# Performance work log

Hardware: AMD Instinct MI355X
Metric: run time of the kernel (lower is better)

Reference implementation:

```python
import jax, jax.numpy as jnp
import numpy as np

B, S, D, H = 2, 2048, 1024, 16
DK = D // H  # 64
ROPE_BASE = 10000.0


def _rope_tables(dk, seq_len, base=ROPE_BASE):
    inv_freq = 1.0 / base ** (jnp.arange(0, dk, 2, dtype=jnp.float32) / dk)
    t = jnp.arange(seq_len, dtype=jnp.float32)
    freqs = t[:, None] * inv_freq[None, :]            # [S, dk/2]
    cos = jnp.repeat(jnp.cos(freqs), 2, axis=-1)      # [S, dk] (repeat_interleave)
    sin = jnp.repeat(jnp.sin(freqs), 2, axis=-1)
    return cos, sin


def _rotate_half(x):
    x1, x2 = jnp.split(x, 2, axis=-1)
    return jnp.concatenate((-x2, x1), axis=-1)


def setup_inputs() -> dict:
    key = jax.random.key(0)
    ks = jax.random.split(key, 9)
    scale = 0.02
    x = jax.random.normal(ks[0], (B, S, D), jnp.float32)
    wq = jax.random.normal(ks[1], (D, D), jnp.float32) * scale
    wk = jax.random.normal(ks[2], (D, D), jnp.float32) * scale
    wv = jax.random.normal(ks[3], (D, D), jnp.float32) * scale
    wo = jax.random.normal(ks[4], (D, D), jnp.float32) * scale
    bq = jnp.zeros((D,), jnp.float32)
    bk = jnp.zeros((D,), jnp.float32)
    bv = jnp.zeros((D,), jnp.float32)
    bo = jnp.zeros((D,), jnp.float32)
    mask = jnp.tril(jnp.ones((S, S), dtype=bool))[None, None]  # [1,1,S,S] causal
    return {"x": x, "mask": mask, "wq": wq, "bq": bq, "wk": wk, "bk": bk,
            "wv": wv, "bv": bv, "wo": wo, "bo": bo}


def reference(x, mask, wq, bq, wk, bk, wv, bv, wo, bo):
    b, s, d = x.shape
    h, dk = H, DK
    # QKV projections (nn.Linear: x @ W^T + b), split heads -> [B,H,S,dk]
    q = (x @ wq.T + bq).reshape(b, s, h, dk).transpose(0, 2, 1, 3)
    k = (x @ wk.T + bk).reshape(b, s, h, dk).transpose(0, 2, 1, 3)
    v = (x @ wv.T + bv).reshape(b, s, h, dk).transpose(0, 2, 1, 3)
    # RoPE
    cos, sin = _rope_tables(dk, s)                    # [S, dk]
    cos = cos[None, None]                             # [1,1,S,dk]
    sin = sin[None, None]
    q = q * cos + _rotate_half(q) * sin
    k = k * cos + _rotate_half(k) * sin
    # Naive attention: full [B,H,S,S] scores
    scores = jnp.einsum("bhqd,bhkd->bhqk", q, k) / np.float32(np.sqrt(dk))
    scores = jnp.where(mask, scores, jnp.float32(-1e9))
    attn = jax.nn.softmax(scores, axis=-1)
    out = jnp.einsum("bhqk,bhkd->bhqd", attn, v)      # [B,H,S,dk]
    out = out.transpose(0, 2, 1, 3).reshape(b, s, d)  # [B,S,D]
    return out @ wo.T + bo
```

## Files before the change

### kernel.cpp

```cpp
#include <hip/hip_runtime.h>
#include <hip/hip_bf16.h>

#define B_ 2
#define S_ 2048
#define D_ 1024
#define H_ 16
#define DK_ 64
#define BH_ (B_*H_)

typedef __attribute__((ext_vector_type(8))) short short8;
typedef __attribute__((ext_vector_type(4))) short short4v;
typedef __attribute__((ext_vector_type(4))) float f32x4;

__device__ __forceinline__ unsigned short f2bf(float f) {
  unsigned u = __float_as_uint(f);
  u += 0x7FFFu + ((u >> 16) & 1u);
  return (unsigned short)(u >> 16);
}
__device__ __forceinline__ float bf2f(unsigned short b) {
  return __uint_as_float(((unsigned)b) << 16);
}
__device__ __forceinline__ unsigned pk2bf(float lo, float hi) {
  float2 f; f.x = lo; f.y = hi;
  __hip_bfloat162 t = __float22bfloat162_rn(f);
  unsigned r; __builtin_memcpy(&r, &t, 4); return r;
}
__device__ __forceinline__ float fexp2(float x) {
  float r; asm("v_exp_f32 %0, %1" : "=v"(r) : "v"(x)); return r;
}

__device__ __forceinline__ long ftile_off(int n, int k, int ktiles) {
  return ((long)(n >> 7) * ktiles + (k >> 5)) * 4096 + ((k >> 3) & 3) * 1024 + (n & 127) * 8 + (k & 7);
}

__global__ __launch_bounds__(256) void cvt_kernel(const float* __restrict__ x, const float* __restrict__ wq,
                           const float* __restrict__ wk, const float* __restrict__ wv,
                           const float* __restrict__ wo, const float* __restrict__ bq,
                           const float* __restrict__ bk, const float* __restrict__ bv,
                           unsigned short* __restrict__ xb, unsigned short* __restrict__ wqkvb,
                           unsigned short* __restrict__ wob, float* __restrict__ bqkv,
                           float* __restrict__ ctab) {
  const int bi = blockIdx.x;
  if (bi >= 2051) {
    const int idx = (bi - 2051) * 256 + (int)threadIdx.x;
    const int s = idx >> 5, j = idx & 31;
    const float invf = fexp2((float)j * -0.4152410118609203f);
    float sn, cc;
    __sincosf((float)s * invf, &sn, &cc);
    ctab[(long)idx * 2] = cc;
    ctab[(long)idx * 2 + 1] = sn;
    return;
  }
  if (bi >= 2048) {
    const int i = (bi - 2048) * 1024 + (int)threadIdx.x * 4;
    const float* bb = (i < D_) ? (bq + i) : ((i < 2 * D_) ? (bk + i - D_) : (bv + i - 2 * D_));
    *(float4*)(bqkv + i) = *(const float4*)bb;
    return;
  }
  __shared__ alignas(16) unsigned short lt[4096];
  const int t = threadIdx.x;
  const int r = t >> 1, kb = (t & 1) * 16;
  int ti; unsigned short* dst;
  if (bi < 1024) { ti = bi; dst = xb; }
  else if (bi < 1792) { ti = bi - 1024; dst = wqkvb; }
  else { ti = bi - 1792; dst = wob; }
  const int rt = ti >> 5, kt = ti & 31;
  const int grow = rt * 128 + r;
  const float* sp;
  if (bi < 1024) sp = x + (long)grow * 1024 + kt * 32 + kb;
  else if (bi < 1792) {
    const float* w = (grow < 1024) ? wq : ((grow < 2048) ? wk : wv);
    sp = w + (long)(grow & 1023) * 1024 + kt * 32 + kb;
  } else sp = wo + (long)grow * 1024 + kt * 32 + kb;

  const float4 va = ((const float4*)sp)[0], vb = ((const float4*)sp)[1];
  const float4 vc = ((const float4*)sp)[2], vd = ((const float4*)sp)[3];
  short8 o0, o1;
  o0[0] = f2bf(va.x); o0[1] = f2bf(va.y); o0[2] = f2bf(va.z); o0[3] = f2bf(va.w);
  o0[4] = f2bf(vb.x); o0[5] = f2bf(vb.y); o0[6] = f2bf(vb.z); o0[7] = f2bf(vb.w);
  o1[0] = f2bf(vc.x); o1[1] = f2bf(vc.y); o1[2] = f2bf(vc.z); o1[3] = f2bf(vc.w);
  o1[4] = f2bf(vd.x); o1[5] = f2bf(vd.y); o1[6] = f2bf(vd.z); o1[7] = f2bf(vd.w);
  const int kc0 = kb >> 3;
  *(short8*)(lt + kc0 * 1024 + r * 8) = o0;
  *(short8*)(lt + (kc0 + 1) * 1024 + r * 8) = o1;
  __syncthreads();
  unsigned short* dp = dst + ((long)rt * 32 + kt) * 4096 + t * 16;
  *(short8*)dp       = *(const short8*)(lt + t * 16);
  *(short8*)(dp + 8) = *(const short8*)(lt + t * 16 + 8);
}

__global__ __launch_bounds__(256) void gemm_qkv(const unsigned short* __restrict__ A,
                                                const unsigned short* __restrict__ Bm,
                                                const float* __restrict__ bias,
                                                const float* __restrict__ ctab,
                                                unsigned short* __restrict__ Qh,
                                                unsigned short* __restrict__ Kf,
                                                unsigned short* __restrict__ Vf) {
  __shared__ alignas(16) unsigned short As[4096];
  __shared__ alignas(16) unsigned short Bs[4096];
  __shared__ alignas(16) unsigned short epi[4 * 4480];
  const int t = threadIdx.x;
  const int w = t >> 6;
  const int lane = t & 63;
  const int bcol = blockIdx.x * 128;
  const int wr = (w >> 1) * 64, wc = (w & 1) * 64;
  const int fr = lane & 15;
  const int g = lane >> 4;
  const int ktiles = 32;
  f32x4 acc[4][4] = {};

  for (int kt = 0; kt < ktiles; ++kt) {
    const unsigned short* Asrc = A  + ((long)blockIdx.y * ktiles + kt) * 4096;
    const unsigned short* Bsrc = Bm + ((long)blockIdx.x * ktiles + kt) * 4096;
#pragma unroll
    for (int j = 0; j < 2; ++j) {
      const int off = (w * 2 + j) * 512;
      __builtin_amdgcn_global_load_lds((const __attribute__((address_space(1))) void*)(Asrc + off + lane * 8),
                                       (__attribute__((address_space(3))) void*)(As + off), 16, 0, 0);
      __builtin_amdgcn_global_load_lds((const __attribute__((address_space(1))) void*)(Bsrc + off + lane * 8),
                                       (__attribute__((address_space(3))) void*)(Bs + off), 16, 0, 0);
    }
    __syncthreads();
    short8 a[4], b[4];
#pragma unroll
    for (int m = 0; m < 4; ++m)
      a[m] = *(const short8*)(As + g * 1024 + (wr + m * 16 + fr) * 8);
#pragma unroll
    for (int n = 0; n < 4; ++n)
      b[n] = *(const short8*)(Bs + g * 1024 + (wc + n * 16 + fr) * 8);
#pragma unroll
    for (int m = 0; m < 4; ++m)
#pragma unroll
      for (int n = 0; n < 4; ++n)
        acc[m][n] = __builtin_amdgcn_mfma_f32_16x16x32_bf16(a[m], b[n], acc[m][n], 0, 0, 0);
    __syncthreads();
  }

  const int colbase = bcol + wc;
  const int ct = colbase >> 6;
  const int h = ct & 15;
  const int rowbase = blockIdx.y * 128 + wr;
  const int s0 = rowbase & (S_ - 1);
  const int bh = (rowbase >> 11) * 16 + h;
  unsigned short* ep = epi + w * 4480;

#pragma unroll
  for (int n = 0; n < 4; ++n) {
    const int d = n * 16 + fr;
    const float bb = bias[colbase + d];
#pragma unroll
    for (int m = 0; m < 4; ++m)
#pragma unroll
      for (int i = 0; i < 4; ++i)
        ep[(m * 16 + g * 4 + i) * 70 + d] = f2bf(acc[m][n][i] + bb);
  }

  if (ct < 32) {
    const bool isQ = (ct < 16);
    const int s = s0 + lane;
    const unsigned short* rp = ep + lane * 70;
    const f32x4* cp4 = (const f32x4*)(ctab + (long)s * 64);
    const float QS = 0.18033688011112043f;
    unsigned short* qp = Qh + (long)bh * (S_ * DK_) + (long)s * DK_;
    unsigned short* kp = Kf + (long)bh * (S_ * DK_) + (long)(s >> 4) * 1024 + (s & 15) * 8;
#pragma unroll
    for (int c = 0; c < 4; ++c) {
      const short8 vlo = *(const short8*)(rp + c * 8);
      const short8 vhi = *(const short8*)(rp + 32 + c * 8);
      const f32x4 tl0 = cp4[c * 2],     tl1 = cp4[c * 2 + 1];
      const f32x4 th0 = cp4[8 + c * 2], th1 = cp4[8 + c * 2 + 1];
      short8 olo, ohi;
#pragma unroll
      for (int e = 0; e < 8; ++e) {
        const int j = e >> 1;
        const float c1 = (j < 2) ? ((j & 1) ? tl0[2] : tl0[0]) : ((j & 1) ? tl1[2] : tl1[0]);
        const float s1 = (j < 2) ? ((j & 1) ? tl0[3] : tl0[1]) : ((j & 1) ? tl1[3] : tl1[1]);
        const float c2 = (j < 2) ? ((j & 1) ? th0[2] : th0[0]) : ((j & 1) ? th1[2] : th1[0]);
        const float s2 = (j < 2) ? ((j & 1) ? th0[3] : th0[1]) : ((j & 1) ? th1[3] : th1[1]);
        const float v1 = bf2f((unsigned short)vlo[e]);
        const float v2 = bf2f((unsigned short)vhi[e]);
        float o1 = v1 * c1 - v2 * s1;
        float o2 = v2 * c2 + v1 * s2;
        if (isQ) { o1 *= QS; o2 *= QS; }
        olo[e] = (short)f2bf(o1);
        ohi[e] = (short)f2bf(o2);
      }
      if (isQ) {
        *(short8*)(qp + c * 8) = olo;
        *(short8*)(qp + 32 + c * 8) = ohi;
      } else {
        *(short8*)(kp + c * 128) = olo;
        *(short8*)(kp + 512 + c * 128) = ohi;
      }
    }
  } else {
#pragma unroll
    for (int c32loc = 0; c32loc < 2; ++c32loc) {
      unsigned short* vb = Vf + ((long)(bh * 64 + (s0 >> 5) + c32loc)) * 2048;
#pragma unroll
      for (int q = 0; q < 4; ++q) {
        const int idx = q * 64 + lane;
        const int tt = idx >> 6, g2 = (idx >> 4) & 3, frd = idx & 15;
        const int d = tt * 16 + frd;
        short8 o;
#pragma unroll
        for (int j = 0; j < 8; ++j) {
          const int r = (j < 4) ? (4 * g2 + j) : (16 + 4 * g2 + (j - 4));
          o[j] = ep[(c32loc * 32 + r) * 70 + d];
        }
        *(short8*)(vb + tt * 512 + g2 * 128 + frd * 8) = o;
      }
    }
  }
}

template<bool OUT_F32>
__global__ __launch_bounds__(256) void gemm_bt(const unsigned short* __restrict__ A,
                                               const unsigned short* __restrict__ Bm,
                                               const float* __restrict__ bias,
                                               void* __restrict__ Cp, int M, int N, int K) {
  __shared__ alignas(16) unsigned short As[4096];
  __shared__ alignas(16) unsigned short Bs[4096];
  const int t = threadIdx.x;
  const int w = t >> 6;
  const int lane = t & 63;
  const int brow = blockIdx.y * 128;
  const int bcol = blockIdx.x * 128;
  const int wr = (w >> 1) * 64, wc = (w & 1) * 64;
  const int fr = lane & 15;
  const int g = lane >> 4;
  const int ktiles = K >> 5;
  f32x4 acc[4][4] = {};

  for (int kt = 0; kt < ktiles; ++kt) {
    const unsigned short* Asrc = A  + ((long)blockIdx.y * ktiles + kt) * 4096;
    const unsigned short* Bsrc = Bm + ((long)blockIdx.x * ktiles + kt) * 4096;
#pragma unroll
    for (int j = 0; j < 2; ++j) {
      const int off = (w * 2 + j) * 512;
      __builtin_amdgcn_global_load_lds((const __attribute__((address_space(1))) void*)(Asrc + off + lane * 8),
                                       (__attribute__((address_space(3))) void*)(As + off), 16, 0, 0);
      __builtin_amdgcn_global_load_lds((const __attribute__((address_space(1))) void*)(Bsrc + off + lane * 8),
                                       (__attribute__((address_space(3))) void*)(Bs + off), 16, 0, 0);
    }
    __syncthreads();
    short8 a[4], b[4];
#pragma unroll
    for (int m = 0; m < 4; ++m)
      a[m] = *(const short8*)(As + g * 1024 + (wr + m * 16 + fr) * 8);
#pragma unroll
    for (int n = 0; n < 4; ++n)
      b[n] = *(const short8*)(Bs + g * 1024 + (wc + n * 16 + fr) * 8);
#pragma unroll
    for (int m = 0; m < 4; ++m)
#pragma unroll
      for (int n = 0; n < 4; ++n)
        acc[m][n] = __builtin_amdgcn_mfma_f32_16x16x32_bf16(a[m], b[n], acc[m][n], 0, 0, 0);
    __syncthreads();
  }

#pragma unroll
  for (int m = 0; m < 4; ++m) {
#pragma unroll
    for (int n = 0; n < 4; ++n) {
      const int col = bcol + wc + n * 16 + fr;
      const float bv_ = bias[col];
#pragma unroll
      for (int i = 0; i < 4; ++i) {
        const int row = brow + wr + m * 16 + g * 4 + i;
        const float v = acc[m][n][i] + bv_;
        if (OUT_F32) ((float*)Cp)[(long)row * N + col] = v;
        else ((unsigned short*)Cp)[(long)row * N + col] = f2bf(v);
      }
    }
  }
}

__global__ __launch_bounds__(256) void flash_kernel(const unsigned short* __restrict__ Qh,
                                                    const unsigned short* __restrict__ Kf,
                                                    const unsigned short* __restrict__ Vf,
                                                    unsigned short* __restrict__ attnout) {
  __shared__ alignas(16) unsigned short Ks[8192];
  __shared__ alignas(16) unsigned short Vs[8192];

  const int flat = (int)blockIdx.x;
  const int xcd = flat & 7;
  const int ix  = flat >> 3;
  const int k   = ix >> 5;
  const int c   = ix & 31;
  const int bh  = xcd * 4 + k;
  const int qblk = (k & 1) ? c : 31 - c;

  const int b = bh >> 4, h = bh & 15;
  const int w = threadIdx.x >> 6, lane = threadIdx.x & 63;
  const int fr = lane & 15, g = lane >> 4;
  const int qg = qblk * 64 + w * 16 + fr;

  const unsigned short* Qb = Qh + (long)bh * (S_ * DK_);
  const short8 qf0 = *(const short8*)(Qb + (long)qg * DK_ + g * 8);
  const short8 qf1 = *(const short8*)(Qb + (long)qg * DK_ + 32 + g * 8);

  short8 vone;
#pragma unroll
  for (int i = 0; i < 8; ++i) vone[i] = (short)0x3F80;

  f32x4 acc[4] = {};
  f32x4 acl = {};

  const unsigned short* kfb = Kf + (long)bh * (S_ * DK_);
  const unsigned short* vfb = Vf + (long)bh * (S_ * DK_);
  const int kvend = qblk * 64;
  const int frag = g * 128 + fr * 8;

  for (int kv0 = 0; kv0 <= kvend; kv0 += 128) {
    {
      const unsigned short* gk = kfb + (long)kv0 * 64 + w * 2048 + lane * 8;
      unsigned short* lk = Ks + w * 2048;
      const unsigned short* gv = vfb + (long)kv0 * 64 + w * 2048 + lane * 8;
      unsigned short* lv = Vs + w * 2048;
#pragma unroll
      for (int cc = 0; cc < 4; ++cc) {
        __builtin_amdgcn_global_load_lds((const __attribute__((address_space(1))) void*)(gk + cc * 512),
                                         (__attribute__((address_space(3))) void*)(lk + cc * 512), 16, 0, 0);
        __builtin_amdgcn_global_load_lds((const __attribute__((address_space(1))) void*)(gv + cc * 512),
                                         (__attribute__((address_space(3))) void*)(lv + cc * 512), 16, 0, 0);
      }
    }
    __syncthreads();
    const bool domask = (kv0 + 128 > kvend);

#pragma unroll
    for (int sub = 0; sub < 2; ++sub) {
      const unsigned short* ksb = Ks + sub * 4096;
      const unsigned short* vsb = Vs + sub * 4096;

      f32x4 st[4];
      __builtin_amdgcn_s_setprio(1);
#pragma unroll
      for (int cc = 0; cc < 4; ++cc) {
        const short8 k0 = *(const short8*)(ksb + cc * 1024 + frag);
        const short8 k1 = *(const short8*)(ksb + cc * 1024 + 512 + frag);
        f32x4 z = {};
        z = __builtin_amdgcn_mfma_f32_16x16x32_bf16(k0, qf0, z, 0, 0, 0);
        z = __builtin_amdgcn_mfma_f32_16x16x32_bf16(k1, qf1, z, 0, 0, 0);
        st[cc] = z;
      }
      __builtin_amdgcn_s_setprio(0);

      if (domask) {
        const int base = kv0 + sub * 64 + g * 4;
#pragma unroll
        for (int cc = 0; cc < 4; ++cc)
#pragma unroll
          for (int i = 0; i < 4; ++i)
            if (base + cc * 16 + i > qg) st[cc][i] = -3.0e38f;
      }

      float ps[16];
#pragma unroll
      for (int cc = 0; cc < 4; ++cc)
#pragma unroll
        for (int i = 0; i < 4; ++i) ps[cc * 4 + i] = fexp2(st[cc][i]);

      union { short8 s8; unsigned u[4]; } P0, P1;
#pragma unroll
      for (int i = 0; i < 4; ++i) {
        P0.u[i] = pk2bf(ps[2 * i], ps[2 * i + 1]);
        P1.u[i] = pk2bf(ps[8 + 2 * i], ps[8 + 2 * i + 1]);
      }

      __builtin_amdgcn_s_setprio(1);
#pragma unroll
      for (int t = 0; t < 4; ++t) {
        const short8 va = *(const short8*)(vsb + t * 512 + frag);
        const short8 vb = *(const short8*)(vsb + 2048 + t * 512 + frag);
        acc[t] = __builtin_amdgcn_mfma_f32_16x16x32_bf16(va, P0.s8, acc[t], 0, 0, 0);
        acc[t] = __builtin_amdgcn_mfma_f32_16x16x32_bf16(vb, P1.s8, acc[t], 0, 0, 0);
      }
      acl = __builtin_amdgcn_mfma_f32_16x16x32_bf16(vone, P0.s8, acl, 0, 0, 0);
      acl = __builtin_amdgcn_mfma_f32_16x16x32_bf16(vone, P1.s8, acl, 0, 0, 0);
      __builtin_amdgcn_s_setprio(0);
    }
    __syncthreads();
  }

  const float ri = 1.0f / acl[0];
  const int row = b * S_ + qg;
#pragma unroll
  for (int t = 0; t < 4; ++t) {
    short4v ov;
#pragma unroll
    for (int i = 0; i < 4; ++i) ov[i] = (short)f2bf(acc[t][i] * ri);
    const int kcol = h * 64 + t * 16 + g * 4;
    *(short4v*)(attnout + ftile_off(row, kcol, 32)) = ov;
  }
}

extern "C" void kernel_launch(void* const* d_in, const int* in_sizes, int n_in,
                              void* d_out, int out_size, void* d_ws, size_t ws_size,
                              hipStream_t stream) {
  const float* x  = (const float*)d_in[0];
  const float* wq = (const float*)d_in[2];
  const float* bq = (const float*)d_in[3];
  const float* wk = (const float*)d_in[4];
  const float* bk = (const float*)d_in[5];
  const float* wv = (const float*)d_in[6];
  const float* bv = (const float*)d_in[7];
  const float* wo = (const float*)d_in[8];
  const float* bo = (const float*)d_in[9];

  const long NX = (long)B_ * S_ * D_;
  const long NW = (long)D_ * D_;

  unsigned short* xb    = (unsigned short*)d_ws;
  unsigned short* wqkvb = xb + NX;
  unsigned short* wob   = wqkvb + 3 * NW;
  float*          bqkv  = (float*)(wob + NW);
  unsigned short* Qh    = (unsigned short*)(bqkv + 3 * D_);
  unsigned short* Kf    = Qh + NX;
  unsigned short* Vf    = Kf + NX;
  float*          ctab  = (float*)(Vf + NX);
  unsigned short* attnout = xb;

  cvt_kernel<<<2307, 256, 0, stream>>>(x, wq, wk, wv, wo, bq, bk, bv,
                                       xb, wqkvb, wob, bqkv, ctab);
  gemm_qkv<<<dim3(24, 32), 256, 0, stream>>>(xb, wqkvb, bqkv, ctab, Qh, Kf, Vf);
  flash_kernel<<<1024, 256, 0, stream>>>(Qh, Kf, Vf, attnout);
  gemm_bt<true><<<dim3(8, 32), 256, 0, stream>>>(attnout, wob, bo, d_out, 4096, 1024, 1024);
}
```

Before: 108.5 us.

## Process two 64-row query tiles per flash block to reuse K/V loads

Each flash-attention block now handles 128 query rows: each wave holds two sets of Q fragments and computes scores for both against every staged K/V chunk. K/V shared-memory traffic per query is halved, and the kernel launches half as many blocks. The grid-to-(bh, qblk) mapping is reworked so long and short causal blocks are paired within an XCD. On the last chunk the A tile skips the second sub-tile, which is fully masked for it. The cost is roughly double the accumulator registers, which may lower occupancy, plus fewer blocks to spread the causal imbalance over.

```diff
diff --git a/kernel.cpp b/kernel.cpp
--- a/kernel.cpp
+++ b/kernel.cpp
@@ -286,33 +286,36 @@
   const int flat = (int)blockIdx.x;
   const int xcd = flat & 7;
   const int ix  = flat >> 3;
-  const int k   = ix >> 5;
+  const int p   = ix >> 5;
   const int c   = ix & 31;
-  const int bh  = xcd * 4 + k;
-  const int qblk = (k & 1) ? c : 31 - c;
+  const int bh  = xcd * 4 + (c & 1) + 2 * p;
+  const int qblk = p ? (15 - (c >> 1)) : (c >> 1);
 
   const int b = bh >> 4, h = bh & 15;
   const int w = threadIdx.x >> 6, lane = threadIdx.x & 63;
   const int fr = lane & 15, g = lane >> 4;
-  const int qg = qblk * 64 + w * 16 + fr;
+  const int qgA = qblk * 128 + w * 16 + fr;
+  const int qgB = qgA + 64;
 
   const unsigned short* Qb = Qh + (long)bh * (S_ * DK_);
-  const short8 qf0 = *(const short8*)(Qb + (long)qg * DK_ + g * 8);
-  const short8 qf1 = *(const short8*)(Qb + (long)qg * DK_ + 32 + g * 8);
+  const short8 qA0 = *(const short8*)(Qb + (long)qgA * DK_ + g * 8);
+  const short8 qA1 = *(const short8*)(Qb + (long)qgA * DK_ + 32 + g * 8);
+  const short8 qB0 = *(const short8*)(Qb + (long)qgB * DK_ + g * 8);
+  const short8 qB1 = *(const short8*)(Qb + (long)qgB * DK_ + 32 + g * 8);
 
   short8 vone;
 #pragma unroll
   for (int i = 0; i < 8; ++i) vone[i] = (short)0x3F80;
 
-  f32x4 acc[4] = {};
-  f32x4 acl = {};
+  f32x4 accA[4] = {}, accB[4] = {};
+  f32x4 aclA = {}, aclB = {};
 
   const unsigned short* kfb = Kf + (long)bh * (S_ * DK_);
   const unsigned short* vfb = Vf + (long)bh * (S_ * DK_);
-  const int kvend = qblk * 64;
+  const int kvlast = qblk * 128;
   const int frag = g * 128 + fr * 8;
 
-  for (int kv0 = 0; kv0 <= kvend; kv0 += 128) {
+  for (int kv0 = 0; kv0 <= kvlast; kv0 += 128) {
     {
       const unsigned short* gk = kfb + (long)kv0 * 64 + w * 2048 + lane * 8;
       unsigned short* lk = Ks + w * 2048;
@@ -327,46 +330,74 @@
       }
     }
     __syncthreads();
-    const bool domask = (kv0 + 128 > kvend);
+    const bool lastchunk = (kv0 == kvlast);
 
 #pragma unroll
     for (int sub = 0; sub < 2; ++sub) {
       const unsigned short* ksb = Ks + sub * 4096;
       const unsigned short* vsb = Vs + sub * 4096;
-
-      f32x4 st[4];
+      const bool doA = !(lastchunk && sub == 1);
+
+      f32x4 stA[4], stB[4];
       __builtin_amdgcn_s_setprio(1);
 #pragma unroll
       for (int cc = 0; cc < 4; ++cc) {
         const short8 k0 = *(const short8*)(ksb + cc * 1024 + frag);
         const short8 k1 = *(const short8*)(ksb + cc * 1024 + 512 + frag);
-        f32x4 z = {};
-        z = __builtin_amdgcn_mfma_f32_16x16x32_bf16(k0, qf0, z, 0, 0, 0);
-        z = __builtin_amdgcn_mfma_f32_16x16x32_bf16(k1, qf1, z, 0, 0, 0);
-        st[cc] = z;
+        if (doA) {
+          f32x4 z = {};
+          z = __builtin_amdgcn_mfma_f32_16x16x32_bf16(k0, qA0, z, 0, 0, 0);
+          z = __builtin_amdgcn_mfma_f32_16x16x32_bf16(k1, qA1, z, 0, 0, 0);
+          stA[cc] = z;
+        }
+        f32x4 y = {};
+        y = __builtin_amdgcn_mfma_f32_16x16x32_bf16(k0, qB0, y, 0, 0, 0);
+        y = __builtin_amdgcn_mfma_f32_16x16x32_bf16(k1, qB1, y, 0, 0, 0);
+        stB[cc] = y;
       }
       __builtin_amdgcn_s_setprio(0);
 
-      if (domask) {
+      if (lastchunk) {
         const int base = kv0 + sub * 64 + g * 4;
+        if (sub == 0) {
+#pragma unroll
+          for (int cc = 0; cc < 4; ++cc)
+#pragma unroll
+            for (int i = 0; i < 4; ++i)
+              if (base + cc * 16 + i > qgA) stA[cc][i] = -3.0e38f;
+        } else {
+#pragma unroll
+          for (int cc = 0; cc < 4; ++cc)
+#pragma unroll
+            for (int i = 0; i < 4; ++i)
+              if (base + cc * 16 + i > qgB) stB[cc][i] = -3.0e38f;
+        }
+      }
+
+      union { short8 s8; unsigned u[4]; } PA0, PA1, PB0, PB1;
+      if (doA) {
+        float ps[16];
 #pragma unroll
         for (int cc = 0; cc < 4; ++cc)
 #pragma unroll
-          for (int i = 0; i < 4; ++i)
-            if (base + cc * 16 + i > qg) st[cc][i] = -3.0e38f;
-      }
-
-      float ps[16];
-#pragma unroll
-      for (int cc = 0; cc < 4; ++cc)
-#pragma unroll
-        for (int i = 0; i < 4; ++i) ps[cc * 4 + i] = fexp2(st[cc][i]);
-
-      union { short8 s8; unsigned u[4]; } P0, P1;
-#pragma unroll
-      for (int i = 0; i < 4; ++i) {
-        P0.u[i] = pk2bf(ps[2 * i], ps[2 * i + 1]);
-        P1.u[i] = pk2bf(ps[8 + 2 * i], ps[8 + 2 * i + 1]);
+          for (int i = 0; i < 4; ++i) ps[cc * 4 + i] = fexp2(stA[cc][i]);
+#pragma unroll
+        for (int i = 0; i < 4; ++i) {
+          PA0.u[i] = pk2bf(ps[2 * i], ps[2 * i + 1]);
+          PA1.u[i] = pk2bf(ps[8 + 2 * i], ps[8 + 2 * i + 1]);
+        }
+      }
+      {
+        float ps[16];
+#pragma unroll
+        for (int cc = 0; cc < 4; ++cc)
+#pragma unroll
+          for (int i = 0; i < 4; ++i) ps[cc * 4 + i] = fexp2(stB[cc][i]);
+#pragma unroll
+        for (int i = 0; i < 4; ++i) {
+          PB0.u[i] = pk2bf(ps[2 * i], ps[2 * i + 1]);
+          PB1.u[i] = pk2bf(ps[8 + 2 * i], ps[8 + 2 * i + 1]);
+        }
       }
 
       __builtin_amdgcn_s_setprio(1);
@@ -374,25 +405,39 @@
       for (int t = 0; t < 4; ++t) {
         const short8 va = *(const short8*)(vsb + t * 512 + frag);
         const short8 vb = *(const short8*)(vsb + 2048 + t * 512 + frag);
-        acc[t] = __builtin_amdgcn_mfma_f32_16x16x32_bf16(va, P0.s8, acc[t], 0, 0, 0);
-        acc[t] = __builtin_amdgcn_mfma_f32_16x16x32_bf16(vb, P1.s8, acc[t], 0, 0, 0);
-      }
-      acl = __builtin_amdgcn_mfma_f32_16x16x32_bf16(vone, P0.s8, acl, 0, 0, 0);
-      acl = __builtin_amdgcn_mfma_f32_16x16x32_bf16(vone, P1.s8, acl, 0, 0, 0);
+        if (doA) {
+          accA[t] = __builtin_amdgcn_mfma_f32_16x16x32_bf16(va, PA0.s8, accA[t], 0, 0, 0);
+          accA[t] = __builtin_amdgcn_mfma_f32_16x16x32_bf16(vb, PA1.s8, accA[t], 0, 0, 0);
+        }
+        accB[t] = __builtin_amdgcn_mfma_f32_16x16x32_bf16(va, PB0.s8, accB[t], 0, 0, 0);
+        accB[t] = __builtin_amdgcn_mfma_f32_16x16x32_bf16(vb, PB1.s8, accB[t], 0, 0, 0);
+      }
+      if (doA) {
+        aclA = __builtin_amdgcn_mfma_f32_16x16x32_bf16(vone, PA0.s8, aclA, 0, 0, 0);
+        aclA = __builtin_amdgcn_mfma_f32_16x16x32_bf16(vone, PA1.s8, aclA, 0, 0, 0);
+      }
+      aclB = __builtin_amdgcn_mfma_f32_16x16x32_bf16(vone, PB0.s8, aclB, 0, 0, 0);
+      aclB = __builtin_amdgcn_mfma_f32_16x16x32_bf16(vone, PB1.s8, aclB, 0, 0, 0);
       __builtin_amdgcn_s_setprio(0);
     }
     __syncthreads();
   }
 
-  const float ri = 1.0f / acl[0];
-  const int row = b * S_ + qg;
+  const float riA = 1.0f / aclA[0];
+  const float riB = 1.0f / aclB[0];
+  const int rowA = b * S_ + qgA;
+  const int rowB = b * S_ + qgB;
 #pragma unroll
   for (int t = 0; t < 4; ++t) {
-    short4v ov;
-#pragma unroll
-    for (int i = 0; i < 4; ++i) ov[i] = (short)f2bf(acc[t][i] * ri);
+    short4v ovA, ovB;
+#pragma unroll
+    for (int i = 0; i < 4; ++i) {
+      ovA[i] = (short)f2bf(accA[t][i] * riA);
+      ovB[i] = (short)f2bf(accB[t][i] * riB);
+    }
     const int kcol = h * 64 + t * 16 + g * 4;
-    *(short4v*)(attnout + ftile_off(row, kcol, 32)) = ov;
+    *(short4v*)(attnout + ftile_off(rowA, kcol, 32)) = ovA;
+    *(short4v*)(attnout + ftile_off(rowB, kcol, 32)) = ovB;
   }
 }
 
@@ -425,6 +470,6 @@
   cvt_kernel<<<2307, 256, 0, stream>>>(x, wq, wk, wv, wo, bq, bk, bv,
                                        xb, wqkvb, wob, bqkv, ctab);
   gemm_qkv<<<dim3(24, 32), 256, 0, stream>>>(xb, wqkvb, bqkv, ctab, Qh, Kf, Vf);
-  flash_kernel<<<1024, 256, 0, stream>>>(Qh, Kf, Vf, attnout);
+  flash_kernel<<<512, 256, 0, stream>>>(Qh, Kf, Vf, attnout);
   gemm_bt<true><<<dim3(8, 32), 256, 0, stream>>>(attnout, wob, bo, d_out, 4096, 1024, 1024);
 }
```

Result: slower. 117.1 us (+7.9%).

## Double-buffer K/V tiles in flash kernel with async prefetch

Applied to the files above, without the earlier changes.

Replaces the single 128-row K/V LDS load per iteration with two 64-row buffers. The next tile is prefetched via global_load_lds while the current one is computed, using explicit vmcnt waits and barriers. This is meant to hide global memory latency behind the MFMA work, at the cost of an extra barrier per 64-row step and a finer loop granularity. The masking condition is simplified to the diagonal tile only.

```diff
diff --git a/kernel.cpp b/kernel.cpp
--- a/kernel.cpp
+++ b/kernel.cpp
@@ -280,8 +280,8 @@
                                                     const unsigned short* __restrict__ Kf,
                                                     const unsigned short* __restrict__ Vf,
                                                     unsigned short* __restrict__ attnout) {
-  __shared__ alignas(16) unsigned short Ks[8192];
-  __shared__ alignas(16) unsigned short Vs[8192];
+  __shared__ alignas(16) unsigned short Ks[2][4096];
+  __shared__ alignas(16) unsigned short Vs[2][4096];
 
   const int flat = (int)blockIdx.x;
   const int xcd = flat & 7;
@@ -296,92 +296,104 @@
   const int fr = lane & 15, g = lane >> 4;
   const int qg = qblk * 64 + w * 16 + fr;
 
-  const unsigned short* Qb = Qh + (long)bh * (S_ * DK_);
-  const short8 qf0 = *(const short8*)(Qb + (long)qg * DK_ + g * 8);
-  const short8 qf1 = *(const short8*)(Qb + (long)qg * DK_ + 32 + g * 8);
-
-  short8 vone;
-#pragma unroll
-  for (int i = 0; i < 8; ++i) vone[i] = (short)0x3F80;
-
-  f32x4 acc[4] = {};
-  f32x4 acl = {};
-
   const unsigned short* kfb = Kf + (long)bh * (S_ * DK_);
   const unsigned short* vfb = Vf + (long)bh * (S_ * DK_);
   const int kvend = qblk * 64;
   const int frag = g * 128 + fr * 8;
 
-  for (int kv0 = 0; kv0 <= kvend; kv0 += 128) {
-    {
-      const unsigned short* gk = kfb + (long)kv0 * 64 + w * 2048 + lane * 8;
-      unsigned short* lk = Ks + w * 2048;
-      const unsigned short* gv = vfb + (long)kv0 * 64 + w * 2048 + lane * 8;
-      unsigned short* lv = Vs + w * 2048;
-#pragma unroll
-      for (int cc = 0; cc < 4; ++cc) {
-        __builtin_amdgcn_global_load_lds((const __attribute__((address_space(1))) void*)(gk + cc * 512),
-                                         (__attribute__((address_space(3))) void*)(lk + cc * 512), 16, 0, 0);
-        __builtin_amdgcn_global_load_lds((const __attribute__((address_space(1))) void*)(gv + cc * 512),
-                                         (__attribute__((address_space(3))) void*)(lv + cc * 512), 16, 0, 0);
-      }
-    }
-    __syncthreads();
-    const bool domask = (kv0 + 128 > kvend);
-
-#pragma unroll
-    for (int sub = 0; sub < 2; ++sub) {
-      const unsigned short* ksb = Ks + sub * 4096;
-      const unsigned short* vsb = Vs + sub * 4096;
-
-      f32x4 st[4];
-      __builtin_amdgcn_s_setprio(1);
-#pragma unroll
-      for (int cc = 0; cc < 4; ++cc) {
-        const short8 k0 = *(const short8*)(ksb + cc * 1024 + frag);
-        const short8 k1 = *(const short8*)(ksb + cc * 1024 + 512 + frag);
-        f32x4 z = {};
-        z = __builtin_amdgcn_mfma_f32_16x16x32_bf16(k0, qf0, z, 0, 0, 0);
-        z = __builtin_amdgcn_mfma_f32_16x16x32_bf16(k1, qf1, z, 0, 0, 0);
-        st[cc] = z;
-      }
-      __builtin_amdgcn_s_setprio(0);
-
-      if (domask) {
-        const int base = kv0 + sub * 64 + g * 4;
-#pragma unroll
-        for (int cc = 0; cc < 4; ++cc)
-#pragma unroll
-          for (int i = 0; i < 4; ++i)
-            if (base + cc * 16 + i > qg) st[cc][i] = -3.0e38f;
-      }
-
-      float ps[16];
+  auto stage = [&](int kv0, int buf) {
+    const unsigned short* gk = kfb + (long)kv0 * 64 + w * 1024 + lane * 8;
+    unsigned short* lk = &Ks[buf][w * 1024];
+    __builtin_amdgcn_global_load_lds((const __attribute__((address_space(1))) void*)gk,
+                                     (__attribute__((address_space(3))) void*)lk, 16, 0, 0);
+    __builtin_amdgcn_global_load_lds((const __attribute__((address_space(1))) void*)(gk + 512),
+                                     (__attribute__((address_space(3))) void*)(lk + 512), 16, 0, 0);
+    const unsigned short* gv = vfb + (long)kv0 * 64 + w * 1024 + lane * 8;
+    unsigned short* lv = &Vs[buf][w * 1024];
+    __builtin_amdgcn_global_load_lds((const __attribute__((address_space(1))) void*)gv,
+                                     (__attribute__((address_space(3))) void*)lv, 16, 0, 0);
+    __builtin_amdgcn_global_load_lds((const __attribute__((address_space(1))) void*)(gv + 512),
+                                     (__attribute__((address_space(3))) void*)(lv + 512), 16, 0, 0);
+  };
+
+  stage(0, 0);
+  if (64 <= kvend) stage(64, 1);
+  const unsigned short* Qb = Qh + (long)bh * (S_ * DK_);
+  const short8 qf0 = *(const short8*)(Qb + (long)qg * DK_ + g * 8);
+  const short8 qf1 = *(const short8*)(Qb + (long)qg * DK_ + 32 + g * 8);
+
+  short8 vone;
+#pragma unroll
+  for (int i = 0; i < 8; ++i) vone[i] = (short)0x3F80;
+
+  f32x4 acc[4] = {};
+  f32x4 acl = {};
+
+  int cur = 0;
+  for (int kv0 = 0; kv0 <= kvend; kv0 += 64) {
+    if (kv0 + 64 <= kvend) {
+      asm volatile("s_waitcnt vmcnt(4)" ::: "memory");
+    } else {
+      asm volatile("s_waitcnt vmcnt(0)" ::: "memory");
+    }
+    __builtin_amdgcn_sched_barrier(0);
+    __builtin_amdgcn_s_barrier();
+
+    const unsigned short* ksb = Ks[cur];
+    const unsigned short* vsb = Vs[cur];
+
+    f32x4 st[4];
+    __builtin_amdgcn_s_setprio(1);
+#pragma unroll
+    for (int cc = 0; cc < 4; ++cc) {
+      const short8 k0 = *(const short8*)(ksb + cc * 1024 + frag);
+      const short8 k1 = *(const short8*)(ksb + cc * 1024 + 512 + frag);
+      f32x4 z = {};
+      z = __builtin_amdgcn_mfma_f32_16x16x32_bf16(k0, qf0, z, 0, 0, 0);
+      z = __builtin_amdgcn_mfma_f32_16x16x32_bf16(k1, qf1, z, 0, 0, 0);
+      st[cc] = z;
+    }
+    __builtin_amdgcn_s_setprio(0);
+
+    if (kv0 == kvend) {
 #pragma unroll
       for (int cc = 0; cc < 4; ++cc)
 #pragma unroll
-        for (int i = 0; i < 4; ++i) ps[cc * 4 + i] = fexp2(st[cc][i]);
-
-      union { short8 s8; unsigned u[4]; } P0, P1;
-#pragma unroll
-      for (int i = 0; i < 4; ++i) {
-        P0.u[i] = pk2bf(ps[2 * i], ps[2 * i + 1]);
-        P1.u[i] = pk2bf(ps[8 + 2 * i], ps[8 + 2 * i + 1]);
-      }
-
-      __builtin_amdgcn_s_setprio(1);
-#pragma unroll
-      for (int t = 0; t < 4; ++t) {
-        const short8 va = *(const short8*)(vsb + t * 512 + frag);
-        const short8 vb = *(const short8*)(vsb + 2048 + t * 512 + frag);
-        acc[t] = __builtin_amdgcn_mfma_f32_16x16x32_bf16(va, P0.s8, acc[t], 0, 0, 0);
-        acc[t] = __builtin_amdgcn_mfma_f32_16x16x32_bf16(vb, P1.s8, acc[t], 0, 0, 0);
-      }
-      acl = __builtin_amdgcn_mfma_f32_16x16x32_bf16(vone, P0.s8, acl, 0, 0, 0);
-      acl = __builtin_amdgcn_mfma_f32_16x16x32_bf16(vone, P1.s8, acl, 0, 0, 0);
-      __builtin_amdgcn_s_setprio(0);
-    }
-    __syncthreads();
+        for (int i = 0; i < 4; ++i)
+          if (kv0 + cc * 16 + g * 4 + i > qg) st[cc][i] = -3.0e38f;
+    }
+
+    float ps[16];
+#pragma unroll
+    for (int cc = 0; cc < 4; ++cc)
+#pragma unroll
+      for (int i = 0; i < 4; ++i) ps[cc * 4 + i] = fexp2(st[cc][i]);
+
+    union { short8 s8; unsigned u[4]; } P0, P1;
+#pragma unroll
+    for (int i = 0; i < 4; ++i) {
+      P0.u[i] = pk2bf(ps[2 * i], ps[2 * i + 1]);
+      P1.u[i] = pk2bf(ps[8 + 2 * i], ps[8 + 2 * i + 1]);
+    }
+
+    __builtin_amdgcn_s_setprio(1);
+#pragma unroll
+    for (int t = 0; t < 4; ++t) {
+      const short8 va = *(const short8*)(vsb + t * 512 + frag);
+      const short8 vb = *(const short8*)(vsb + 2048 + t * 512 + frag);
+      acc[t] = __builtin_amdgcn_mfma_f32_16x16x32_bf16(va, P0.s8, acc[t], 0, 0, 0);
+      acc[t] = __builtin_amdgcn_mfma_f32_16x16x32_bf16(vb, P1.s8, acc[t], 0, 0, 0);
+    }
+    acl = __builtin_amdgcn_mfma_f32_16x16x32_bf16(vone, P0.s8, acl, 0, 0, 0);
+    acl = __builtin_amdgcn_mfma_f32_16x16x32_bf16(vone, P1.s8, acl, 0, 0, 0);
+    __builtin_amdgcn_s_setprio(0);
+
+    asm volatile("s_waitcnt lgkmcnt(0)" ::: "memory");
+    __builtin_amdgcn_sched_barrier(0);
+    __builtin_amdgcn_s_barrier();
+
+    if (kv0 + 128 <= kvend) stage(kv0 + 128, cur);
+    cur ^= 1;
   }
 
   const float ri = 1.0f / acl[0];
```

Result: no change. 109.3 us (+0.8%).
